# Kernel optimization log

Hardware: AMD Instinct MI355X
Metric: run time of the kernel (lower is better)

The kernel has to match this reference:

```python
import jax, jax.numpy as jnp
import numpy as np

NUM_HEADS = 16
HEAD_DIM = 64
SCALE = HEAD_DIM ** -0.5


def setup_inputs() -> dict:
    key = jax.random.key(0)
    ks = jax.random.split(key, 5)
    B, N, C = 2, 2048, 1024
    x = jax.random.normal(ks[0], (B, N, C), dtype=jnp.float32)
    rel_pos_bias = jax.random.normal(ks[1], (NUM_HEADS, N, N), dtype=jnp.float32) * 0.02
    qkv_w = jax.random.normal(ks[2], (3 * C, C), dtype=jnp.float32) * (C ** -0.5)
    q_bias = jnp.zeros((C,), dtype=jnp.float32)
    v_bias = jnp.zeros((C,), dtype=jnp.float32)
    proj_w = jax.random.normal(ks[3], (C, C), dtype=jnp.float32) * (C ** -0.5)
    proj_b = jnp.zeros((C,), dtype=jnp.float32)
    return {"x": x, "rel_pos_bias": rel_pos_bias, "qkv_w": qkv_w,
            "q_bias": q_bias, "v_bias": v_bias, "proj_w": proj_w, "proj_b": proj_b}


def reference(x, rel_pos_bias, qkv_w, q_bias, v_bias, proj_w, proj_b):
    B, N, C = x.shape
    H, D = NUM_HEADS, HEAD_DIM
    # qkv bias = concat(q_bias, zeros, v_bias)
    qkv_b = jnp.concatenate([q_bias, jnp.zeros_like(v_bias), v_bias])
    qkv = x @ qkv_w.T + qkv_b                       # [B, N, 3C]
    qkv = qkv.reshape(B, N, 3, H, D).transpose(2, 0, 3, 1, 4)  # [3, B, H, N, D]
    q, k, v = qkv[0], qkv[1], qkv[2]
    q = q * SCALE
    attn = jnp.einsum('bhnd,bhmd->bhnm', q, k)      # [B, H, N, N]
    attn = attn + rel_pos_bias[None]                # bias broadcast over batch
    attn = jax.nn.softmax(attn, axis=-1)
    out = jnp.einsum('bhnm,bhmd->bhnd', attn, v)    # [B, H, N, D]
    out = out.transpose(0, 2, 1, 3).reshape(B, N, H * D)
    out = out @ proj_w.T + proj_b
    return out
```

## Files before the change

kernel.cpp:

```cpp
#include <hip/hip_runtime.h>

typedef unsigned short u16;
typedef short bfrag __attribute__((ext_vector_type(8)));
typedef float facc  __attribute__((ext_vector_type(4)));

#define LOG2E 1.44269504088896340736f

static __device__ __forceinline__ float bf2f(u16 b) {
  union { unsigned u; float f; } v; v.u = ((unsigned)b) << 16; return v.f;
}
static __device__ __forceinline__ u16 f2bf(float x) {
  union { float f; unsigned u; } v; v.f = x;
  return (u16)((v.u + 0x7FFFu + ((v.u >> 16) & 1u)) >> 16);
}
static __device__ __forceinline__ void gload_lds16(const u16* g, u16* l) {
  __builtin_amdgcn_global_load_lds((const __attribute__((address_space(1))) void*)g,
                                   (__attribute__((address_space(3))) void*)l,
                                   16, 0, 0);
}

__global__ __launch_bounds__(256) void convert_kernel(
    const float* __restrict__ x, const float* __restrict__ qw, const float* __restrict__ pw,
    u16* __restrict__ xb, u16* __restrict__ qwb, u16* __restrict__ pwb)
{
  const int NX = 4 * 1024 * 1024, NQ = 3 * 1024 * 1024, NP = 1024 * 1024;
  const int total4 = (NX + NQ + NP) >> 2;
  for (int i = blockIdx.x * blockDim.x + threadIdx.x; i < total4;
       i += gridDim.x * blockDim.x) {
    const int e = i << 2;
    const float* s; u16* d; int off;
    if (e < NX)            { s = x;  d = xb;  off = e; }
    else if (e < NX + NQ)  { s = qw; d = qwb; off = e - NX; }
    else                   { s = pw; d = pwb; off = e - NX - NQ; }
    float4 v = *(const float4*)(s + off);
    ushort4 o;
    o.x = f2bf(v.x); o.y = f2bf(v.y); o.z = f2bf(v.z); o.w = f2bf(v.w);
    *(ushort4*)(d + off) = o;
  }
}

static __device__ __forceinline__ void gemm128_bt(
    const u16* __restrict__ A, const u16* __restrict__ B, int K,
    int m0, int n0, u16* As, u16* Bs, facc acc[4][4])
{
  const int lane = threadIdx.x & 63;
  const int wv   = threadIdx.x >> 6;
  const int quad = lane >> 4;
  const int l15  = lane & 15;
  const int wm = wv >> 1, wn = wv & 1;
  const int srow = lane >> 2;
  const int skb  = (lane & 3) * 8;

  facc zero = {0.f, 0.f, 0.f, 0.f};
#pragma unroll
  for (int i = 0; i < 4; ++i)
#pragma unroll
    for (int j = 0; j < 4; ++j) acc[i][j] = zero;

  const int nIter = K >> 5;
  for (int kk = 0; kk < nIter; ++kk) {
    const int k0 = kk << 5;
    __syncthreads();
#pragma unroll
    for (int c = 0; c < 2; ++c) {
      const int seg = wv * 2 + c;
      gload_lds16(A + (long)(m0 + seg * 16 + srow) * K + k0 + skb, As + seg * 512);
      gload_lds16(B + (long)(n0 + seg * 16 + srow) * K + k0 + skb, Bs + seg * 512);
    }
    __syncthreads();
    bfrag af[4], bf[4];
#pragma unroll
    for (int i = 0; i < 4; ++i)
      af[i] = *(const bfrag*)(As + (wm * 64 + i * 16 + l15) * 32 + quad * 8);
#pragma unroll
    for (int j = 0; j < 4; ++j)
      bf[j] = *(const bfrag*)(Bs + (wn * 64 + j * 16 + l15) * 32 + quad * 8);
#pragma unroll
    for (int i = 0; i < 4; ++i)
#pragma unroll
      for (int j = 0; j < 4; ++j)
        acc[i][j] = __builtin_amdgcn_mfma_f32_16x16x32_bf16(af[i], bf[j], acc[i][j], 0, 0, 0);
  }
}

__global__ __launch_bounds__(256) void qkv_gemm_kernel(
    const u16* __restrict__ x, const u16* __restrict__ w,
    const float* __restrict__ qb, const float* __restrict__ vb,
    u16* __restrict__ Q, u16* __restrict__ Kd, u16* __restrict__ Vt)
{
  __shared__ u16 As[128 * 32];
  __shared__ u16 Bs[128 * 32];
  facc acc[4][4];
  const int m0 = blockIdx.y * 128;
  const int n0 = blockIdx.x * 128;
  gemm128_bt(x, w, 1024, m0, n0, As, Bs, acc);

  const int lane = threadIdx.x & 63;
  const int wv = threadIdx.x >> 6;
  const int quad = lane >> 4, l15 = lane & 15;
  const int wm = wv >> 1, wn = wv & 1;
  const int ncb = n0 + wn * 64;
  const int which = ncb >> 10;
  const int h = (ncb >> 6) & 15;

#pragma unroll
  for (int j = 0; j < 4; ++j) {
    const int d = j * 16 + l15;
    const int n_g = ncb + d;
#pragma unroll
    for (int i = 0; i < 4; ++i) {
      const int mg0 = m0 + wm * 64 + i * 16 + quad * 4;
      const int b  = mg0 >> 11;
      const int ns = mg0 & 2047;
      if (which == 0) {
        const float qbv = qb[n_g];
#pragma unroll
        for (int r = 0; r < 4; ++r)
          Q[(((long)(b * 16 + h) * 2048 + ns + r) << 6) + d] =
              f2bf((acc[i][j][r] + qbv) * 0.125f);
      } else if (which == 1) {
#pragma unroll
        for (int r = 0; r < 4; ++r)
          Kd[(((long)(b * 16 + h) * 2048 + ns + r) << 6) + d] = f2bf(acc[i][j][r]);
      } else {
        const float vbv = vb[n_g - 2048];
        ushort4 pk;
        pk.x = f2bf(acc[i][j][0] + vbv);
        pk.y = f2bf(acc[i][j][1] + vbv);
        pk.z = f2bf(acc[i][j][2] + vbv);
        pk.w = f2bf(acc[i][j][3] + vbv);
        *(ushort4*)(Vt + (((long)((b * 16 + h) * 64 + d)) << 11) + ns) = pk;
      }
    }
  }
}

__global__ __launch_bounds__(256) void attn_kernel(
    const u16* __restrict__ Q, const u16* __restrict__ Kd, const u16* __restrict__ Vt,
    const float* __restrict__ bias, u16* __restrict__ AO)
{
  __shared__ u16 P[4][16 * 32];
  const int lane = threadIdx.x & 63;
  const int wv = threadIdx.x >> 6;
  const int quad = lane >> 4, l15 = lane & 15;
  const int bh = blockIdx.x >> 5;
  const int qt = blockIdx.x & 31;
  const int h = bh & 15;
  const int b = bh >> 4;
  const int q0 = qt * 64 + wv * 16;
  const long baseN = (long)bh << 17;

  bfrag qf0 = *(const bfrag*)(Q + baseN + (long)(q0 + l15) * 64 + quad * 8);
  bfrag qf1 = *(const bfrag*)(Q + baseN + (long)(q0 + l15) * 64 + 32 + quad * 8);

  facc o[4];
  float m_i[4], l_i[4];
  facc zero = {0.f, 0.f, 0.f, 0.f};
#pragma unroll
  for (int t = 0; t < 4; ++t) o[t] = zero;
#pragma unroll
  for (int r = 0; r < 4; ++r) { m_i[r] = -1e30f; l_i[r] = 0.f; }

  const float* brow = bias + ((long)h << 22) + ((long)q0 << 11);
  u16* Pw = &P[wv][0];

  for (int k0 = 0; k0 < 2048; k0 += 32) {
    facc s[2];
#pragma unroll
    for (int kt = 0; kt < 2; ++kt) {
      bfrag kf0 = *(const bfrag*)(Kd + baseN + (long)(k0 + kt * 16 + l15) * 64 + quad * 8);
      bfrag kf1 = *(const bfrag*)(Kd + baseN + (long)(k0 + kt * 16 + l15) * 64 + 32 + quad * 8);
      facc z = zero;
      z = __builtin_amdgcn_mfma_f32_16x16x32_bf16(qf0, kf0, z, 0, 0, 0);
      z = __builtin_amdgcn_mfma_f32_16x16x32_bf16(qf1, kf1, z, 0, 0, 0);
      s[kt] = z;
    }
#pragma unroll
    for (int kt = 0; kt < 2; ++kt)
#pragma unroll
      for (int r = 0; r < 4; ++r)
        s[kt][r] += brow[(long)(quad * 4 + r) * 2048 + k0 + kt * 16 + l15];

    float alpha[4];
#pragma unroll
    for (int r = 0; r < 4; ++r) {
      float v = fmaxf(s[0][r], s[1][r]);
      v = fmaxf(v, __shfl_xor(v, 1, 16));
      v = fmaxf(v, __shfl_xor(v, 2, 16));
      v = fmaxf(v, __shfl_xor(v, 4, 16));
      v = fmaxf(v, __shfl_xor(v, 8, 16));
      const float mn = fmaxf(m_i[r], v);
      alpha[r] = exp2f((m_i[r] - mn) * LOG2E);
      m_i[r] = mn;
    }
#pragma unroll
    for (int r = 0; r < 4; ++r) {
      const float p0 = exp2f((s[0][r] - m_i[r]) * LOG2E);
      const float p1 = exp2f((s[1][r] - m_i[r]) * LOG2E);
      s[0][r] = p0; s[1][r] = p1;
      float v = p0 + p1;
      v += __shfl_xor(v, 1, 16);
      v += __shfl_xor(v, 2, 16);
      v += __shfl_xor(v, 4, 16);
      v += __shfl_xor(v, 8, 16);
      l_i[r] = l_i[r] * alpha[r] + v;
    }
#pragma unroll
    for (int t = 0; t < 4; ++t)
#pragma unroll
      for (int r = 0; r < 4; ++r) o[t][r] *= alpha[r];

#pragma unroll
    for (int kt = 0; kt < 2; ++kt)
#pragma unroll
      for (int r = 0; r < 4; ++r)
        Pw[(quad * 4 + r) * 32 + kt * 16 + l15] = f2bf(s[kt][r]);
    __syncthreads();

    bfrag pf = *(const bfrag*)(Pw + l15 * 32 + quad * 8);
#pragma unroll
    for (int t = 0; t < 4; ++t) {
      bfrag vf = *(const bfrag*)(Vt + baseN + (((long)(t * 16 + l15)) << 11) + k0 + quad * 8);
      o[t] = __builtin_amdgcn_mfma_f32_16x16x32_bf16(pf, vf, o[t], 0, 0, 0);
    }
    __syncthreads();
  }

#pragma unroll
  for (int r = 0; r < 4; ++r) l_i[r] = 1.0f / l_i[r];
#pragma unroll
  for (int t = 0; t < 4; ++t)
#pragma unroll
    for (int r = 0; r < 4; ++r) {
      const int row = q0 + quad * 4 + r;
      AO[(((long)(b * 2048 + row)) << 10) + h * 64 + t * 16 + l15] = f2bf(o[t][r] * l_i[r]);
    }
}

__global__ __launch_bounds__(256) void proj_kernel(
    const u16* __restrict__ Ain, const u16* __restrict__ w,
    const float* __restrict__ pb, float* __restrict__ out)
{
  __shared__ u16 As[128 * 32];
  __shared__ u16 Bs[128 * 32];
  facc acc[4][4];
  const int m0 = blockIdx.y * 128;
  const int n0 = blockIdx.x * 128;
  gemm128_bt(Ain, w, 1024, m0, n0, As, Bs, acc);

  const int lane = threadIdx.x & 63;
  const int wv = threadIdx.x >> 6;
  const int quad = lane >> 4, l15 = lane & 15;
  const int wm = wv >> 1, wn = wv & 1;
#pragma unroll
  for (int j = 0; j < 4; ++j) {
    const int n_g = n0 + wn * 64 + j * 16 + l15;
    const float pbv = pb[n_g];
#pragma unroll
    for (int i = 0; i < 4; ++i) {
      const int mg0 = m0 + wm * 64 + i * 16 + quad * 4;
#pragma unroll
      for (int r = 0; r < 4; ++r)
        out[(((long)(mg0 + r)) << 10) + n_g] = acc[i][j][r] + pbv;
    }
  }
}

extern "C" void kernel_launch(void* const* d_in, const int* in_sizes, int n_in,
                              void* d_out, int out_size, void* d_ws, size_t ws_size,
                              hipStream_t stream)
{
  const float* x    = (const float*)d_in[0];
  const float* bias = (const float*)d_in[1];
  const float* qkvw = (const float*)d_in[2];
  const float* qb   = (const float*)d_in[3];
  const float* vb   = (const float*)d_in[4];
  const float* pw   = (const float*)d_in[5];
  const float* pb   = (const float*)d_in[6];
  float* out = (float*)d_out;

  char* ws = (char*)d_ws;
  u16* Q    = (u16*)(ws);
  u16* Kd   = (u16*)(ws + (size_t)8  * 1024 * 1024);
  u16* Vt   = (u16*)(ws + (size_t)16 * 1024 * 1024);
  u16* AO   = (u16*)(ws + (size_t)24 * 1024 * 1024);
  u16* xb   = (u16*)(ws + (size_t)32 * 1024 * 1024);
  u16* qwb  = (u16*)(ws + (size_t)40 * 1024 * 1024);
  u16* pwb  = (u16*)(ws + (size_t)46 * 1024 * 1024);

  hipLaunchKernelGGL(convert_kernel, dim3(1024), dim3(256), 0, stream,
                     x, qkvw, pw, xb, qwb, pwb);
  hipLaunchKernelGGL(qkv_gemm_kernel, dim3(24, 32), dim3(256), 0, stream,
                     xb, qwb, qb, vb, Q, Kd, Vt);
  hipLaunchKernelGGL(attn_kernel, dim3(1024), dim3(256), 0, stream,
                     Q, Kd, Vt, bias, AO);
  hipLaunchKernelGGL(proj_kernel, dim3(8, 32), dim3(256), 0, stream,
                     AO, pwb, pb, out);
}
```

Before: 642.3 us.

## Widen attention KV tile, prefetch bias in registers, swizzle P LDS, drop barriers

The attention inner loop now processes 64 keys per iteration instead of 32, so there are fewer online-softmax rescales and loop overheads per key. The relative-position bias for the next tile is prefetched into registers with nontemporal loads during the current tile, hiding the latency of this large streamed read. The per-wave P buffer uses an XOR-swizzled layout to avoid LDS bank conflicts. The block-wide __syncthreads are removed because each wave only touches its own P slice. The trade-off is higher register pressure from the bias, V-fragment and score arrays, which may reduce occupancy.

```diff
diff --git a/kernel.cpp b/kernel.cpp
--- a/kernel.cpp
+++ b/kernel.cpp
@@ -139,7 +139,7 @@
     const u16* __restrict__ Q, const u16* __restrict__ Kd, const u16* __restrict__ Vt,
     const float* __restrict__ bias, u16* __restrict__ AO)
 {
-  __shared__ u16 P[4][16 * 32];
+  __shared__ u16 P[4][16 * 64];
   const int lane = threadIdx.x & 63;
   const int wv = threadIdx.x >> 6;
   const int quad = lane >> 4, l15 = lane & 15;
@@ -162,29 +162,38 @@
   for (int r = 0; r < 4; ++r) { m_i[r] = -1e30f; l_i[r] = 0.f; }
 
   const float* brow = bias + ((long)h << 22) + ((long)q0 << 11);
-  u16* Pw = &P[wv][0];
-
-  for (int k0 = 0; k0 < 2048; k0 += 32) {
-    facc s[2];
-#pragma unroll
-    for (int kt = 0; kt < 2; ++kt) {
-      bfrag kf0 = *(const bfrag*)(Kd + baseN + (long)(k0 + kt * 16 + l15) * 64 + quad * 8);
-      bfrag kf1 = *(const bfrag*)(Kd + baseN + (long)(k0 + kt * 16 + l15) * 64 + 32 + quad * 8);
+  char* PwB = (char*)&P[wv][0];
+
+  float bn[16];
+#pragma unroll
+  for (int kt = 0; kt < 4; ++kt)
+#pragma unroll
+    for (int r = 0; r < 4; ++r)
+      bn[kt * 4 + r] =
+          __builtin_nontemporal_load(brow + (long)(quad * 4 + r) * 2048 + kt * 16 + l15);
+
+  for (int k0 = 0; k0 < 2048; k0 += 64) {
+    facc s[4];
+#pragma unroll
+    for (int kt = 0; kt < 4; ++kt) {
+      const u16* kb = Kd + baseN + (long)(k0 + kt * 16 + l15) * 64;
+      bfrag kf0 = *(const bfrag*)(kb + quad * 8);
+      bfrag kf1 = *(const bfrag*)(kb + 32 + quad * 8);
       facc z = zero;
       z = __builtin_amdgcn_mfma_f32_16x16x32_bf16(qf0, kf0, z, 0, 0, 0);
       z = __builtin_amdgcn_mfma_f32_16x16x32_bf16(qf1, kf1, z, 0, 0, 0);
       s[kt] = z;
     }
 #pragma unroll
-    for (int kt = 0; kt < 2; ++kt)
+    for (int kt = 0; kt < 4; ++kt)
 #pragma unroll
       for (int r = 0; r < 4; ++r)
-        s[kt][r] += brow[(long)(quad * 4 + r) * 2048 + k0 + kt * 16 + l15];
+        s[kt][r] += bn[kt * 4 + r];
 
     float alpha[4];
 #pragma unroll
     for (int r = 0; r < 4; ++r) {
-      float v = fmaxf(s[0][r], s[1][r]);
+      float v = fmaxf(fmaxf(s[0][r], s[1][r]), fmaxf(s[2][r], s[3][r]));
       v = fmaxf(v, __shfl_xor(v, 1, 16));
       v = fmaxf(v, __shfl_xor(v, 2, 16));
       v = fmaxf(v, __shfl_xor(v, 4, 16));
@@ -197,8 +206,10 @@
     for (int r = 0; r < 4; ++r) {
       const float p0 = exp2f((s[0][r] - m_i[r]) * LOG2E);
       const float p1 = exp2f((s[1][r] - m_i[r]) * LOG2E);
-      s[0][r] = p0; s[1][r] = p1;
-      float v = p0 + p1;
+      const float p2 = exp2f((s[2][r] - m_i[r]) * LOG2E);
+      const float p3 = exp2f((s[3][r] - m_i[r]) * LOG2E);
+      s[0][r] = p0; s[1][r] = p1; s[2][r] = p2; s[3][r] = p3;
+      float v = (p0 + p1) + (p2 + p3);
       v += __shfl_xor(v, 1, 16);
       v += __shfl_xor(v, 2, 16);
       v += __shfl_xor(v, 4, 16);
@@ -211,19 +222,46 @@
       for (int r = 0; r < 4; ++r) o[t][r] *= alpha[r];
 
 #pragma unroll
-    for (int kt = 0; kt < 2; ++kt)
-#pragma unroll
-      for (int r = 0; r < 4; ++r)
-        Pw[(quad * 4 + r) * 32 + kt * 16 + l15] = f2bf(s[kt][r]);
-    __syncthreads();
-
-    bfrag pf = *(const bfrag*)(Pw + l15 * 32 + quad * 8);
+    for (int kt = 0; kt < 4; ++kt)
+#pragma unroll
+      for (int r = 0; r < 4; ++r) {
+        const int row = quad * 4 + r;
+        int bo = row * 128 + (kt * 16 + l15) * 2;
+        bo ^= (row & 7) << 4;
+        *(u16*)(PwB + bo) = f2bf(s[kt][r]);
+      }
+
+    bfrag pf[2];
+#pragma unroll
+    for (int p = 0; p < 2; ++p) {
+      int bo = l15 * 128 + p * 64 + quad * 16;
+      bo ^= (l15 & 7) << 4;
+      pf[p] = *(const bfrag*)(PwB + bo);
+    }
+
+    bfrag vfr[4][2];
 #pragma unroll
     for (int t = 0; t < 4; ++t) {
-      bfrag vf = *(const bfrag*)(Vt + baseN + (((long)(t * 16 + l15)) << 11) + k0 + quad * 8);
-      o[t] = __builtin_amdgcn_mfma_f32_16x16x32_bf16(pf, vf, o[t], 0, 0, 0);
-    }
-    __syncthreads();
+      const u16* vrow = Vt + baseN + (((long)(t * 16 + l15)) << 11) + k0;
+#pragma unroll
+      for (int p = 0; p < 2; ++p)
+        vfr[t][p] = *(const bfrag*)(vrow + p * 32 + quad * 8);
+    }
+    if (k0 + 64 < 2048) {
+      const float* bnx = brow + k0 + 64;
+#pragma unroll
+      for (int kt = 0; kt < 4; ++kt)
+#pragma unroll
+        for (int r = 0; r < 4; ++r)
+          bn[kt * 4 + r] =
+              __builtin_nontemporal_load(bnx + (long)(quad * 4 + r) * 2048 + kt * 16 + l15);
+    }
+
+#pragma unroll
+    for (int t = 0; t < 4; ++t)
+#pragma unroll
+      for (int p = 0; p < 2; ++p)
+        o[t] = __builtin_amdgcn_mfma_f32_16x16x32_bf16(pf[p], vfr[t][p], o[t], 0, 0, 0);
   }
 
 #pragma unroll
```

Measured after the change: 734.3 us. 14.3% more time.
